# Optimization experiments

Measured on AMD Instinct MI355X. Metric: run time of the kernel, lower is better.

## Reference

```python
import jax, jax.numpy as jnp
import numpy as np

B, N, D = 8, 512, 768
HS = 64          # gp_head_size
NT = 12          # len(tag_vocab)
NEG = 1e12


def setup_inputs() -> dict:
    key = jax.random.key(0)
    ks = jax.random.split(key, 14)
    s = 0.02  # init scale for weights
    return {
        "chars": jax.random.normal(ks[0], (B, N, D), dtype=jnp.float32),
        "mask": jax.random.randint(ks[1], (B, N), 0, 2).astype(jnp.int32),
        "w1_ent": jax.random.normal(ks[2], (2 * HS, D), dtype=jnp.float32) * s,
        "b1_ent": jax.random.normal(ks[3], (2 * HS,), dtype=jnp.float32) * s,
        "w2_ent": jax.random.normal(ks[4], (2 * 2, 2 * HS), dtype=jnp.float32) * s,
        "b2_ent": jax.random.normal(ks[5], (2 * 2,), dtype=jnp.float32) * s,
        "w1_head": jax.random.normal(ks[6], (2 * HS, D), dtype=jnp.float32) * s,
        "b1_head": jax.random.normal(ks[7], (2 * HS,), dtype=jnp.float32) * s,
        "w2_head": jax.random.normal(ks[8], (2 * NT, 2 * HS), dtype=jnp.float32) * s,
        "b2_head": jax.random.normal(ks[9], (2 * NT,), dtype=jnp.float32) * s,
        "w1_tail": jax.random.normal(ks[10], (2 * HS, D), dtype=jnp.float32) * s,
        "b1_tail": jax.random.normal(ks[11], (2 * HS,), dtype=jnp.float32) * s,
        "w2_tail": jax.random.normal(ks[12], (2 * NT, 2 * HS), dtype=jnp.float32) * s,
        "b2_tail": jax.random.normal(ks[13], (2 * NT,), dtype=jnp.float32) * s,
    }


def _egp(x, w1, b1, w2, b2, mask, head_size, rope, tril):
    # x: [B,N,D] -> h: [B,N,2*head_size]
    h = jnp.einsum('bnd,ed->bne', x, w1) + b1
    qw, kw = h[..., 0::2], h[..., 1::2]          # [B,N,head_size] each
    if rope:
        n = x.shape[1]
        pos = jnp.arange(n, dtype=x.dtype)
        inv = jnp.power(10000.0, -2.0 * jnp.arange(head_size // 2, dtype=x.dtype) / head_size)
        ang = pos[:, None] * inv[None, :]         # [N, head_size/2]
        cos = jnp.repeat(jnp.cos(ang), 2, axis=-1)[None]  # [1,N,head_size]
        sin = jnp.repeat(jnp.sin(ang), 2, axis=-1)[None]
        def rot(t):
            t2 = jnp.stack([-t[..., 1::2], t[..., 0::2]], axis=-1).reshape(t.shape)
            return t * cos + t2 * sin
        qw, kw = rot(qw), rot(kw)
    logits = jnp.einsum('bmd,bnd->bmn', qw, kw) / (head_size ** 0.5)  # [B,M,N]
    bias = (jnp.einsum('bne,he->bnh', h, w2) + b2).transpose(0, 2, 1) / 2.0  # [B,2H,N]
    # [B,H,M,N]
    logits = logits[:, None] + bias[:, 0::2, None, :] + bias[:, 1::2, :, None]
    m = mask.astype(logits.dtype)
    pad = 1.0 - m[:, None, None, :] * m[:, None, :, None]
    logits = logits - pad * NEG
    if tril:
        tri = jnp.tril(jnp.ones((logits.shape[-2], logits.shape[-1]), logits.dtype), k=-1)
        logits = logits - tri * NEG
    return logits


def reference(chars, mask, w1_ent, b1_ent, w2_ent, b2_ent,
              w1_head, b1_head, w2_head, b2_head,
              w1_tail, b1_tail, w2_tail, b2_tail):
    entity = _egp(chars, w1_ent, b1_ent, w2_ent, b2_ent, mask, HS, True, True)
    head = _egp(chars, w1_head, b1_head, w2_head, b2_head, mask, HS, False, False)
    tail = _egp(chars, w1_tail, b1_tail, w2_tail, b2_tail, mask, HS, False, False)
    return (entity, head, tail)
```

## Files before the change

kernel.cpp:

```cpp
#include <hip/hip_runtime.h>
#include <cstddef>

namespace {
constexpr int B_ = 8;
constexpr int N_ = 512;
constexpr int D_ = 768;
constexpr int HS_ = 64;
constexpr int M_ = B_ * N_;
constexpr int E_ = 2 * HS_;
constexpr float NEGV = 1000000000000.0f;
constexpr float LOG2_10000 = 13.287712379549449f;
}

template <int H2>
__device__ __forceinline__ void bias_from_lds(
    const float (*hs)[132], const float* __restrict__ w2,
    const float* __restrict__ b2, float* __restrict__ bout,
    int m0, int t)
{
    const int bb = m0 >> 9;
    const int nbase = m0 & 511;
    for (int idx = t; idx < 32 * H2; idx += 256) {
        const int row = idx / H2;
        const int h2  = idx - row * H2;
        const float* w = w2 + (size_t)h2 * E_;
        float s = 0.0f;
        #pragma unroll 8
        for (int e4 = 0; e4 < 32; ++e4) {
            const float4 hv = *(const float4*)&hs[row][4 * e4];
            const float4 wv = *(const float4*)(w + 4 * e4);
            s += hv.x * wv.x + hv.y * wv.y + hv.z * wv.z + hv.w * wv.w;
        }
        s = (s + b2[h2]) * 0.5f;
        bout[((size_t)bb * H2 + h2) * N_ + nbase + row] = s;
    }
}

__global__ __launch_bounds__(256) void prep_kernel(
    const float* __restrict__ chars,
    const float* __restrict__ w1e, const float* __restrict__ b1e,
    const float* __restrict__ w2e, const float* __restrict__ b2e,
    const float* __restrict__ w1h, const float* __restrict__ b1h,
    const float* __restrict__ w2h, const float* __restrict__ b2h,
    const float* __restrict__ w1t, const float* __restrict__ b1t,
    const float* __restrict__ w2t, const float* __restrict__ b2t,
    float* __restrict__ h_base,
    float* __restrict__ bias_e, float* __restrict__ bias_h, float* __restrict__ bias_t)
{
    const int fam = blockIdx.y;
    const float* w1 = (fam == 0) ? w1e : (fam == 1) ? w1h : w1t;
    const float* b1 = (fam == 0) ? b1e : (fam == 1) ? b1h : b1t;
    float* hout = h_base + (size_t)fam * M_ * E_;
    const int m0 = blockIdx.x * 32;

    __shared__ float As[32][33];
    __shared__ float Ws[32][128];
    __shared__ float hs[32][132];

    const int t  = threadIdx.x;
    const int rg = t >> 5;
    const int cg = t & 31;

    float acc[4][4] = {};

    for (int k0 = 0; k0 < D_; k0 += 32) {
        {
            const int ar = t >> 3;
            const int ac = t & 7;
            const float4 v = *(const float4*)(chars + (size_t)(m0 + ar) * D_ + k0 + ac * 4);
            As[ar][ac * 4 + 0] = v.x;
            As[ar][ac * 4 + 1] = v.y;
            As[ar][ac * 4 + 2] = v.z;
            As[ar][ac * 4 + 3] = v.w;
        }
        {
            const int col  = t >> 1;
            const int half = t & 1;
            const float* wp = w1 + (size_t)col * D_ + k0 + half * 16;
            #pragma unroll
            for (int qq = 0; qq < 4; ++qq) {
                const float4 v = *(const float4*)(wp + qq * 4);
                const int kk = half * 16 + qq * 4;
                Ws[kk + 0][col] = v.x;
                Ws[kk + 1][col] = v.y;
                Ws[kk + 2][col] = v.z;
                Ws[kk + 3][col] = v.w;
            }
        }
        __syncthreads();
        #pragma unroll 8
        for (int k = 0; k < 32; ++k) {
            const float a0 = As[rg * 4 + 0][k];
            const float a1 = As[rg * 4 + 1][k];
            const float a2 = As[rg * 4 + 2][k];
            const float a3 = As[rg * 4 + 3][k];
            const float4 wv = *(const float4*)&Ws[k][cg * 4];
            acc[0][0] += a0 * wv.x; acc[0][1] += a0 * wv.y; acc[0][2] += a0 * wv.z; acc[0][3] += a0 * wv.w;
            acc[1][0] += a1 * wv.x; acc[1][1] += a1 * wv.y; acc[1][2] += a1 * wv.z; acc[1][3] += a1 * wv.w;
            acc[2][0] += a2 * wv.x; acc[2][1] += a2 * wv.y; acc[2][2] += a2 * wv.z; acc[2][3] += a2 * wv.w;
            acc[3][0] += a3 * wv.x; acc[3][1] += a3 * wv.y; acc[3][2] += a3 * wv.z; acc[3][3] += a3 * wv.w;
        }
        __syncthreads();
    }

    const float4 bv = *(const float4*)(b1 + cg * 4);
    #pragma unroll
    for (int j = 0; j < 4; ++j) {
        const float4 o = make_float4(acc[j][0] + bv.x, acc[j][1] + bv.y,
                                     acc[j][2] + bv.z, acc[j][3] + bv.w);
        *(float4*)(hout + (size_t)(m0 + rg * 4 + j) * E_ + cg * 4) = o;
        *(float4*)&hs[rg * 4 + j][cg * 4] = o;
    }
    __syncthreads();

    if (fam == 0)      bias_from_lds<4 >(hs, w2e, b2e, bias_e, m0, t);
    else if (fam == 1) bias_from_lds<24>(hs, w2h, b2h, bias_h, m0, t);
    else               bias_from_lds<24>(hs, w2t, b2t, bias_t, m0, t);
}

template <int H, bool ROPE, bool TRIL>
__device__ __forceinline__ void egp_tile(
    const float* __restrict__ hfam, const float* __restrict__ biasfam,
    const int* __restrict__ mask, float* __restrict__ out,
    int b, int m0, int n0, float (*qtT)[68], float (*kt)[68], int t)
{
    const int srow = t >> 2;
    const int sch  = t & 3;

    {
        const float* hq = hfam + (size_t)(b * N_ + m0 + srow) * E_;
        const float* hk = hfam + (size_t)(b * N_ + n0 + srow) * E_;
        #pragma unroll
        for (int jj = 0; jj < 8; ++jj) {
            const int i = sch + 4 * jj;
            const float4 v = *(const float4*)(hq + 4 * i);
            const float4 w = *(const float4*)(hk + 4 * i);
            if (ROPE) {
                const float inv = exp2f(-(float)i * (LOG2_10000 / 32.0f));
                float sq, cq, sk, ck;
                sincosf((float)(m0 + srow) * inv, &sq, &cq);
                sincosf((float)(n0 + srow) * inv, &sk, &ck);
                qtT[2 * i + 0][srow] = v.x * cq - v.z * sq;
                qtT[2 * i + 1][srow] = v.z * cq + v.x * sq;
                kt [2 * i + 0][srow] = w.y * ck - w.w * sk;
                kt [2 * i + 1][srow] = w.w * ck + w.y * sk;
            } else {
                qtT[2 * i + 0][srow] = v.x;
                qtT[2 * i + 1][srow] = v.z;
                kt [2 * i + 0][srow] = w.y;
                kt [2 * i + 1][srow] = w.w;
            }
        }
    }
    __syncthreads();

    const int rq = t >> 4;
    const int cq = t & 15;

    float acc[4][4] = {};
    #pragma unroll 8
    for (int k = 0; k < 64; ++k) {
        const float4 av = *(const float4*)&qtT[k][4 * rq];
        const float4 kv = *(const float4*)&kt [k][4 * cq];
        acc[0][0] += av.x * kv.x; acc[0][1] += av.x * kv.y; acc[0][2] += av.x * kv.z; acc[0][3] += av.x * kv.w;
        acc[1][0] += av.y * kv.x; acc[1][1] += av.y * kv.y; acc[1][2] += av.y * kv.z; acc[1][3] += av.y * kv.w;
        acc[2][0] += av.z * kv.x; acc[2][1] += av.z * kv.y; acc[2][2] += av.z * kv.z; acc[2][3] += av.z * kv.w;
        acc[3][0] += av.w * kv.x; acc[3][1] += av.w * kv.y; acc[3][2] += av.w * kv.z; acc[3][3] += av.w * kv.w;
    }

    #pragma unroll
    for (int j = 0; j < 4; ++j)
        #pragma unroll
        for (int q = 0; q < 4; ++q) acc[j][q] *= 0.125f;

    int mrow[4], mm[4];
    #pragma unroll
    for (int j = 0; j < 4; ++j) {
        mrow[j] = m0 + 4 * rq + j;
        mm[j]   = mask[b * N_ + mrow[j]];
    }
    const int ncol = n0 + 4 * cq;
    const int4 mnv = *(const int4*)(mask + b * N_ + ncol);
    const int mn[4] = { mnv.x, mnv.y, mnv.z, mnv.w };

    #pragma unroll
    for (int hh = 0; hh < H; ++hh) {
        const float4 be = *(const float4*)(biasfam + ((size_t)b * 2 * H + 2 * hh) * N_ + ncol);
        float bo[4];
        #pragma unroll
        for (int j = 0; j < 4; ++j)
            bo[j] = biasfam[((size_t)b * 2 * H + 2 * hh + 1) * N_ + mrow[j]];

        #pragma unroll
        for (int j = 0; j < 4; ++j) {
            float o[4] = { acc[j][0] + be.x + bo[j], acc[j][1] + be.y + bo[j],
                           acc[j][2] + be.z + bo[j], acc[j][3] + be.w + bo[j] };
            #pragma unroll
            for (int q = 0; q < 4; ++q) {
                if (!(mm[j] & mn[q])) o[q] -= NEGV;
                if (TRIL && (ncol + q) < mrow[j]) o[q] -= NEGV;
            }
            *(float4*)(out + ((size_t)(b * H + hh) * N_ + mrow[j]) * N_ + ncol) =
                make_float4(o[0], o[1], o[2], o[3]);
        }
    }
}

__global__ __launch_bounds__(256) void egp_all_kernel(
    const float* __restrict__ h_base,
    const float* __restrict__ bias_e, const float* __restrict__ bias_h,
    const float* __restrict__ bias_t,
    const int* __restrict__ mask, float* __restrict__ out)
{
    __shared__ float qtT[64][68];
    __shared__ float kt [64][68];

    const int t   = threadIdx.x;
    const int m0  = blockIdx.x * 64;
    const int n0  = blockIdx.y * 64;
    const int fam = blockIdx.z >> 3;
    const int b   = blockIdx.z & 7;

    const size_t ent_sz  = (size_t)B_ * 2 * N_ * N_;
    const size_t head_sz = (size_t)B_ * 12 * N_ * N_;

    if (fam == 0) {
        egp_tile<2, true, true>(h_base, bias_e, mask, out, b, m0, n0, qtT, kt, t);
    } else if (fam == 1) {
        egp_tile<12, false, false>(h_base + (size_t)M_ * E_, bias_h, mask,
                                   out + ent_sz, b, m0, n0, qtT, kt, t);
    } else {
        egp_tile<12, false, false>(h_base + (size_t)2 * M_ * E_, bias_t, mask,
                                   out + ent_sz + head_sz, b, m0, n0, qtT, kt, t);
    }
}

extern "C" void kernel_launch(void* const* d_in, const int* in_sizes, int n_in,
                              void* d_out, int out_size, void* d_ws, size_t ws_size,
                              hipStream_t stream)
{
    const float* chars = (const float*)d_in[0];
    const int*   mask  = (const int*)d_in[1];
    const float* w1e = (const float*)d_in[2];
    const float* b1e = (const float*)d_in[3];
    const float* w2e = (const float*)d_in[4];
    const float* b2e = (const float*)d_in[5];
    const float* w1h = (const float*)d_in[6];
    const float* b1h = (const float*)d_in[7];
    const float* w2h = (const float*)d_in[8];
    const float* b2h = (const float*)d_in[9];
    const float* w1t = (const float*)d_in[10];
    const float* b1t = (const float*)d_in[11];
    const float* w2t = (const float*)d_in[12];
    const float* b2t = (const float*)d_in[13];

    float* out = (float*)d_out;

    float* h_ws   = (float*)d_ws;
    float* bias_e = h_ws + (size_t)3 * M_ * E_;
    float* bias_h = bias_e + (size_t)B_ * 4 * N_;
    float* bias_t = bias_h + (size_t)B_ * 24 * N_;

    prep_kernel<<<dim3(M_ / 32, 3), 256, 0, stream>>>(
        chars, w1e, b1e, w2e, b2e, w1h, b1h, w2h, b2h, w1t, b1t, w2t, b2t,
        h_ws, bias_e, bias_h, bias_t);

    egp_all_kernel<<<dim3(8, 8, 24), 256, 0, stream>>>(
        h_ws, bias_e, bias_h, bias_t, mask, out);
}
```

Measured before the change: 318.5 us.

## Use bf16 MFMA for the projection GEMM in the prep kernel

Rewrites the prep kernel's x·W1 projection to convert fp32 inputs to bf16 (by truncation) and run it on MFMA 16x16x32 instructions with 64-row tiles. Global loads for the next K-step are issued into registers before the MFMA work, so they overlap compute. The bias projection is reorganised so each thread owns one row and several output heads. This targets the fp32 FMA cost of the projection GEMM, but lowers input precision to bf16 and halves the grid to 192 blocks, which could leave compute units idle.

```diff
diff --git a/kernel.cpp b/kernel.cpp
--- a/kernel.cpp
+++ b/kernel.cpp
@@ -12,28 +12,12 @@
 constexpr float LOG2_10000 = 13.287712379549449f;
 }
 
-template <int H2>
-__device__ __forceinline__ void bias_from_lds(
-    const float (*hs)[132], const float* __restrict__ w2,
-    const float* __restrict__ b2, float* __restrict__ bout,
-    int m0, int t)
-{
-    const int bb = m0 >> 9;
-    const int nbase = m0 & 511;
-    for (int idx = t; idx < 32 * H2; idx += 256) {
-        const int row = idx / H2;
-        const int h2  = idx - row * H2;
-        const float* w = w2 + (size_t)h2 * E_;
-        float s = 0.0f;
-        #pragma unroll 8
-        for (int e4 = 0; e4 < 32; ++e4) {
-            const float4 hv = *(const float4*)&hs[row][4 * e4];
-            const float4 wv = *(const float4*)(w + 4 * e4);
-            s += hv.x * wv.x + hv.y * wv.y + hv.z * wv.z + hv.w * wv.w;
-        }
-        s = (s + b2[h2]) * 0.5f;
-        bout[((size_t)bb * H2 + h2) * N_ + nbase + row] = s;
-    }
+typedef short mfrag_t __attribute__((ext_vector_type(8)));
+typedef float macc_t  __attribute__((ext_vector_type(4)));
+
+__device__ __forceinline__ unsigned short bft(float x) {
+    union { float f; unsigned u; } c; c.f = x;
+    return (unsigned short)(c.u >> 16);
 }
 
 __global__ __launch_bounds__(256) void prep_kernel(
@@ -50,72 +34,129 @@
     const int fam = blockIdx.y;
     const float* w1 = (fam == 0) ? w1e : (fam == 1) ? w1h : w1t;
     const float* b1 = (fam == 0) ? b1e : (fam == 1) ? b1h : b1t;
+    const float* w2 = (fam == 0) ? w2e : (fam == 1) ? w2h : w2t;
+    const float* b2 = (fam == 0) ? b2e : (fam == 1) ? b2h : b2t;
+    float* bout = (fam == 0) ? bias_e : (fam == 1) ? bias_h : bias_t;
+    const int H2 = (fam == 0) ? 4 : 24;
     float* hout = h_base + (size_t)fam * M_ * E_;
-    const int m0 = blockIdx.x * 32;
-
-    __shared__ float As[32][33];
-    __shared__ float Ws[32][128];
-    __shared__ float hs[32][132];
-
-    const int t  = threadIdx.x;
-    const int rg = t >> 5;
-    const int cg = t & 31;
-
-    float acc[4][4] = {};
-
-    for (int k0 = 0; k0 < D_; k0 += 32) {
+    const int m0 = blockIdx.x * 64;
+
+    __shared__ unsigned short A_lds[64][40];
+    __shared__ unsigned short B_lds[128][40];
+    __shared__ float hs[64][132];
+
+    const int t    = threadIdx.x;
+    const int w    = t >> 6;
+    const int lane = t & 63;
+    const int ml   = lane & 15;
+    const int quad = lane >> 4;
+
+    const int ar = t >> 2;
+    const int ak = (t & 3) * 8;
+    const int bc = t >> 1;
+    const int bk = (t & 1) * 16;
+
+    const float* aptr = chars + (size_t)(m0 + ar) * D_ + ak;
+    const float* bptr = w1 + (size_t)bc * D_ + bk;
+
+    macc_t acc[8];
+    #pragma unroll
+    for (int f = 0; f < 8; ++f) acc[f] = (macc_t)0.0f;
+
+    float4 av0 = *(const float4*)(aptr);
+    float4 av1 = *(const float4*)(aptr + 4);
+    float4 bv0 = *(const float4*)(bptr);
+    float4 bv1 = *(const float4*)(bptr + 4);
+    float4 bv2 = *(const float4*)(bptr + 8);
+    float4 bv3 = *(const float4*)(bptr + 12);
+
+    for (int s = 0; s < 24; ++s) {
         {
-            const int ar = t >> 3;
-            const int ac = t & 7;
-            const float4 v = *(const float4*)(chars + (size_t)(m0 + ar) * D_ + k0 + ac * 4);
-            As[ar][ac * 4 + 0] = v.x;
-            As[ar][ac * 4 + 1] = v.y;
-            As[ar][ac * 4 + 2] = v.z;
-            As[ar][ac * 4 + 3] = v.w;
-        }
-        {
-            const int col  = t >> 1;
-            const int half = t & 1;
-            const float* wp = w1 + (size_t)col * D_ + k0 + half * 16;
-            #pragma unroll
-            for (int qq = 0; qq < 4; ++qq) {
-                const float4 v = *(const float4*)(wp + qq * 4);
-                const int kk = half * 16 + qq * 4;
-                Ws[kk + 0][col] = v.x;
-                Ws[kk + 1][col] = v.y;
-                Ws[kk + 2][col] = v.z;
-                Ws[kk + 3][col] = v.w;
+            mfrag_t pa;
+            pa[0] = (short)bft(av0.x); pa[1] = (short)bft(av0.y);
+            pa[2] = (short)bft(av0.z); pa[3] = (short)bft(av0.w);
+            pa[4] = (short)bft(av1.x); pa[5] = (short)bft(av1.y);
+            pa[6] = (short)bft(av1.z); pa[7] = (short)bft(av1.w);
+            *(mfrag_t*)&A_lds[ar][ak] = pa;
+            mfrag_t pb0, pb1;
+            pb0[0] = (short)bft(bv0.x); pb0[1] = (short)bft(bv0.y);
+            pb0[2] = (short)bft(bv0.z); pb0[3] = (short)bft(bv0.w);
+            pb0[4] = (short)bft(bv1.x); pb0[5] = (short)bft(bv1.y);
+            pb0[6] = (short)bft(bv1.z); pb0[7] = (short)bft(bv1.w);
+            pb1[0] = (short)bft(bv2.x); pb1[1] = (short)bft(bv2.y);
+            pb1[2] = (short)bft(bv2.z); pb1[3] = (short)bft(bv2.w);
+            pb1[4] = (short)bft(bv3.x); pb1[5] = (short)bft(bv3.y);
+            pb1[6] = (short)bft(bv3.z); pb1[7] = (short)bft(bv3.w);
+            *(mfrag_t*)&B_lds[bc][bk]     = pb0;
+            *(mfrag_t*)&B_lds[bc][bk + 8] = pb1;
+        }
+        __syncthreads();
+        if (s < 23) {
+            aptr += 32; bptr += 32;
+            av0 = *(const float4*)(aptr);
+            av1 = *(const float4*)(aptr + 4);
+            bv0 = *(const float4*)(bptr);
+            bv1 = *(const float4*)(bptr + 4);
+            bv2 = *(const float4*)(bptr + 8);
+            bv3 = *(const float4*)(bptr + 12);
+        }
+        const mfrag_t afrag = *(const mfrag_t*)&A_lds[w * 16 + ml][quad * 8];
+        #pragma unroll
+        for (int f = 0; f < 8; ++f) {
+            const mfrag_t bfrag = *(const mfrag_t*)&B_lds[f * 16 + ml][quad * 8];
+            acc[f] = __builtin_amdgcn_mfma_f32_16x16x32_bf16(afrag, bfrag, acc[f], 0, 0, 0);
+        }
+        __syncthreads();
+    }
+
+    #pragma unroll
+    for (int f = 0; f < 8; ++f) {
+        const int col = f * 16 + ml;
+        const float bb1 = b1[col];
+        #pragma unroll
+        for (int r = 0; r < 4; ++r)
+            hs[w * 16 + quad * 4 + r][col] = acc[f][r] + bb1;
+    }
+    __syncthreads();
+
+    {
+        const int row = t >> 2;
+        const int c0  = (t & 3) * 32;
+        float* hp = hout + (size_t)(m0 + row) * E_ + c0;
+        #pragma unroll
+        for (int q = 0; q < 8; ++q)
+            *(float4*)(hp + 4 * q) = *(const float4*)&hs[row][c0 + 4 * q];
+    }
+
+    {
+        const int row = t & 63;
+        const int h2b = t >> 6;
+        const int P   = H2 >> 2;
+        const int bb  = m0 >> 9;
+        const int nb  = (m0 & 511) + row;
+        float accv[6] = {0, 0, 0, 0, 0, 0};
+        for (int e0 = 0; e0 < E_; e0 += 16) {
+            float4 hv0 = *(const float4*)&hs[row][e0];
+            float4 hv1 = *(const float4*)&hs[row][e0 + 4];
+            float4 hv2 = *(const float4*)&hs[row][e0 + 8];
+            float4 hv3 = *(const float4*)&hs[row][e0 + 12];
+            for (int p = 0; p < P; ++p) {
+                const float* wr = w2 + (size_t)(h2b + 4 * p) * E_ + e0;
+                const float4 w0 = *(const float4*)(wr);
+                const float4 w1v = *(const float4*)(wr + 4);
+                const float4 w2v = *(const float4*)(wr + 8);
+                const float4 w3v = *(const float4*)(wr + 12);
+                accv[p] += hv0.x * w0.x + hv0.y * w0.y + hv0.z * w0.z + hv0.w * w0.w
+                         + hv1.x * w1v.x + hv1.y * w1v.y + hv1.z * w1v.z + hv1.w * w1v.w
+                         + hv2.x * w2v.x + hv2.y * w2v.y + hv2.z * w2v.z + hv2.w * w2v.w
+                         + hv3.x * w3v.x + hv3.y * w3v.y + hv3.z * w3v.z + hv3.w * w3v.w;
             }
         }
-        __syncthreads();
-        #pragma unroll 8
-        for (int k = 0; k < 32; ++k) {
-            const float a0 = As[rg * 4 + 0][k];
-            const float a1 = As[rg * 4 + 1][k];
-            const float a2 = As[rg * 4 + 2][k];
-            const float a3 = As[rg * 4 + 3][k];
-            const float4 wv = *(const float4*)&Ws[k][cg * 4];
-            acc[0][0] += a0 * wv.x; acc[0][1] += a0 * wv.y; acc[0][2] += a0 * wv.z; acc[0][3] += a0 * wv.w;
-            acc[1][0] += a1 * wv.x; acc[1][1] += a1 * wv.y; acc[1][2] += a1 * wv.z; acc[1][3] += a1 * wv.w;
-            acc[2][0] += a2 * wv.x; acc[2][1] += a2 * wv.y; acc[2][2] += a2 * wv.z; acc[2][3] += a2 * wv.w;
-            acc[3][0] += a3 * wv.x; acc[3][1] += a3 * wv.y; acc[3][2] += a3 * wv.z; acc[3][3] += a3 * wv.w;
-        }
-        __syncthreads();
-    }
-
-    const float4 bv = *(const float4*)(b1 + cg * 4);
-    #pragma unroll
-    for (int j = 0; j < 4; ++j) {
-        const float4 o = make_float4(acc[j][0] + bv.x, acc[j][1] + bv.y,
-                                     acc[j][2] + bv.z, acc[j][3] + bv.w);
-        *(float4*)(hout + (size_t)(m0 + rg * 4 + j) * E_ + cg * 4) = o;
-        *(float4*)&hs[rg * 4 + j][cg * 4] = o;
-    }
-    __syncthreads();
-
-    if (fam == 0)      bias_from_lds<4 >(hs, w2e, b2e, bias_e, m0, t);
-    else if (fam == 1) bias_from_lds<24>(hs, w2h, b2h, bias_h, m0, t);
-    else               bias_from_lds<24>(hs, w2t, b2t, bias_t, m0, t);
+        for (int p = 0; p < P; ++p) {
+            const int h2 = h2b + 4 * p;
+            bout[((size_t)bb * H2 + h2) * N_ + nb] = (accv[p] + b2[h2]) * 0.5f;
+        }
+    }
 }
 
 template <int H, bool ROPE, bool TRIL>
@@ -261,7 +302,7 @@
     float* bias_h = bias_e + (size_t)B_ * 4 * N_;
     float* bias_t = bias_h + (size_t)B_ * 24 * N_;
 
-    prep_kernel<<<dim3(M_ / 32, 3), 256, 0, stream>>>(
+    prep_kernel<<<dim3(64, 3), 256, 0, stream>>>(
         chars, w1e, b1e, w2e, b2e, w1h, b1h, w2h, b2h, w1t, b1t, w2t, b2t,
         h_ws, bias_e, bias_h, bias_t);
 
```

Result: faster. 297.3 us (-6.7%).
